# Performance work log

Hardware: AMD Instinct MI355X
Metric: run time of the kernel (lower is better)

Reference implementation:

```python
import jax, jax.numpy as jnp
import numpy as np

LN_EPS = 1e-5      # torch.nn.LayerNorm default
NORM_EPS = 1e-12   # torch F.normalize default


def _layernorm(x, gamma, beta):
    mu = jnp.mean(x, axis=-1, keepdims=True)
    var = jnp.mean(jnp.square(x - mu), axis=-1, keepdims=True)
    return (x - mu) * jax.lax.rsqrt(var + LN_EPS) * gamma + beta


def _l2norm(x):
    # normalize over last (embedding) axis, matching F.normalize(dim=1) on [B,E,1,N]
    n = jnp.sqrt(jnp.sum(jnp.square(x), axis=-1, keepdims=True))
    return x / jnp.maximum(n, NORM_EPS)


def setup_inputs() -> dict:
    key = jax.random.key(0)
    ks = jax.random.split(key, 4)
    B, N, C, E = 8, 4096, 768, 768
    x = jax.random.normal(ks[0], (B, N, C), dtype=jnp.float32)
    w_qkv = jax.random.normal(ks[1], (C, 3 * E), dtype=jnp.float32) * (1.0 / np.sqrt(C))
    w_proj = jax.random.normal(ks[2], (E, C), dtype=jnp.float32) * (1.0 / np.sqrt(E))
    ln_in_g = jnp.ones((C,), jnp.float32)
    ln_in_b = jnp.zeros((C,), jnp.float32)
    ln_out_g = jnp.ones((E,), jnp.float32)
    ln_out_b = jnp.zeros((E,), jnp.float32)
    return {"x": x, "w_qkv": w_qkv, "w_proj": w_proj,
            "ln_in_g": ln_in_g, "ln_in_b": ln_in_b,
            "ln_out_g": ln_out_g, "ln_out_b": ln_out_b}


def reference(x, w_qkv, w_proj, ln_in_g, ln_in_b, ln_out_g, ln_out_b):
    # x: [B, N, C]
    h = _layernorm(x, ln_in_g, ln_in_b)
    qkv = h @ w_qkv                                  # [B, N, 3E]
    q, k, v = jnp.split(qkv, 3, axis=-1)             # each [B, N, E]
    phi_q = _l2norm(q)                               # per-token L2 over E
    phi_k = _l2norm(k)
    kv = jnp.sum(phi_k * v, axis=1)                  # [B, E] (sum over tokens N)
    attn = phi_q * kv[:, None, :]                    # [B, N, E]
    out = _layernorm(attn, ln_out_g, ln_out_b) @ w_proj  # [B, N, C]
    return out
```

## Files before the change

### kernel.cpp

```cpp
#include <hip/hip_runtime.h>
#include <hip/hip_bf16.h>
#include <cstdint>

typedef __bf16 bf16;
typedef __bf16 bf16x4 __attribute__((ext_vector_type(4)));
typedef __bf16 bf16x8 __attribute__((ext_vector_type(8)));
typedef float f32x4 __attribute__((ext_vector_type(4)));

#define GK 768
#define LN_EPS 1e-5f
#define NORM_EPS 1e-12f

__device__ __forceinline__ void gl_lds16(const void* g, void* l) {
  __builtin_amdgcn_global_load_lds(
      (__attribute__((address_space(1))) uint32_t*)(uintptr_t)g,
      (__attribute__((address_space(3))) uint32_t*)(uintptr_t)l,
      16, 0, 0);
}

__device__ __forceinline__ void blockReduce2(float& s, float& ss, float* sm) {
  #pragma unroll
  for (int o = 32; o > 0; o >>= 1) {
    s  += __shfl_down(s, o, 64);
    ss += __shfl_down(ss, o, 64);
  }
  int wave = threadIdx.x >> 6, lane = threadIdx.x & 63;
  if (lane == 0) { sm[wave] = s; sm[4 + wave] = ss; }
  __syncthreads();
  s  = sm[0] + sm[1] + sm[2] + sm[3];
  ss = sm[4] + sm[5] + sm[6] + sm[7];
  __syncthreads();
}

__global__ __launch_bounds__(256) void transpose_cvt(const float* __restrict__ w,
                                                     bf16* __restrict__ wt,
                                                     int R, int Ncols) {
  __shared__ float tile[32][33];
  int tx = threadIdx.x & 31, ty = threadIdx.x >> 5;
  int c0 = blockIdx.x * 32, r0 = blockIdx.y * 32;
  #pragma unroll
  for (int i = 0; i < 32; i += 8)
    tile[ty + i][tx] = w[(size_t)(r0 + ty + i) * Ncols + (c0 + tx)];
  __syncthreads();
  #pragma unroll
  for (int i = 0; i < 32; i += 8)
    wt[(size_t)(c0 + ty + i) * R + (r0 + tx)] = (bf16)tile[tx][ty + i];
}

__global__ __launch_bounds__(256) void ln_in_kernel(const float* __restrict__ x,
                                                    const float* __restrict__ g,
                                                    const float* __restrict__ b,
                                                    bf16* __restrict__ h) {
  __shared__ float sm[8];
  int row = blockIdx.x, t = threadIdx.x;
  const float* xr = x + (size_t)row * 768;
  float4 v = make_float4(0.f, 0.f, 0.f, 0.f);
  if (t < 192) v = ((const float4*)xr)[t];
  float s  = v.x + v.y + v.z + v.w;
  float ss = v.x * v.x + v.y * v.y + v.z * v.z + v.w * v.w;
  blockReduce2(s, ss, sm);
  float mu  = s * (1.0f / 768.0f);
  float inv = rsqrtf(ss * (1.0f / 768.0f) - mu * mu + LN_EPS);
  if (t < 192) {
    float4 gg = ((const float4*)g)[t];
    float4 bb = ((const float4*)b)[t];
    bf16x4 o;
    o[0] = (bf16)((v.x - mu) * inv * gg.x + bb.x);
    o[1] = (bf16)((v.y - mu) * inv * gg.y + bb.y);
    o[2] = (bf16)((v.z - mu) * inv * gg.z + bb.z);
    o[3] = (bf16)((v.w - mu) * inv * gg.w + bb.w);
    ((bf16x4*)(h + (size_t)row * 768))[t] = o;
  }
}


#define SWZ(x) ((x) ^ ((((x) >> 7) & 7) << 4))

#define PH_ENTER do { __builtin_amdgcn_sched_barrier(0); __builtin_amdgcn_s_barrier(); \
                      __builtin_amdgcn_sched_barrier(0); } while (0)
#define PH_EXIT  do { __builtin_amdgcn_sched_barrier(0); __builtin_amdgcn_s_barrier(); \
                      __builtin_amdgcn_sched_barrier(0); } while (0)
#define PH_EXIT_V do { __builtin_amdgcn_sched_barrier(0); \
                       asm volatile("s_waitcnt vmcnt(4)" ::: "memory"); \
                       __builtin_amdgcn_s_barrier(); \
                       __builtin_amdgcn_sched_barrier(0); } while (0)

#define LDA1(base, mh, i, ks) \
  af[i][ks] = *(const bf16x8*)((base) + SWZ((wm * 128 + ((mh) * 4 + (i)) * 16 + llo) * 128 + (ks) * 64 + lhi * 16))
#define LDAQ(base, mh) do { \
  LDA1(base, mh, 0, 0); LDA1(base, mh, 0, 1); LDA1(base, mh, 1, 0); LDA1(base, mh, 1, 1); \
  LDA1(base, mh, 2, 0); LDA1(base, mh, 2, 1); LDA1(base, mh, 3, 0); LDA1(base, mh, 3, 1); } while (0)

#define LDB1(base, n, ks) \
  bf[n][ks] = *(const bf16x8*)((base) + SWZ(((((n) >> 1) * 128 + wn * 32 + ((n) & 1) * 16 + llo) * 128 + (ks) * 64 + lhi * 16)))
#define LDBH(base, nlo) do { \
  LDB1(base, nlo, 0); LDB1(base, nlo, 1); LDB1(base, (nlo) + 1, 0); LDB1(base, (nlo) + 1, 1); } while (0)

#define MF1(mh, nh, i, jn, ks) \
  acc[(mh) * 4 + (i)][(nh) * 2 + (jn)] = __builtin_amdgcn_mfma_f32_16x16x32_bf16( \
      af[i][ks], bf[(nh) * 2 + (jn)][ks], acc[(mh) * 4 + (i)][(nh) * 2 + (jn)], 0, 0, 0)
#define MFQ(mh, nh) do { \
  __builtin_amdgcn_s_setprio(1); \
  MF1(mh, nh, 0, 0, 0); MF1(mh, nh, 0, 1, 0); MF1(mh, nh, 1, 0, 0); MF1(mh, nh, 1, 1, 0); \
  MF1(mh, nh, 2, 0, 0); MF1(mh, nh, 2, 1, 0); MF1(mh, nh, 3, 0, 0); MF1(mh, nh, 3, 1, 0); \
  MF1(mh, nh, 0, 0, 1); MF1(mh, nh, 0, 1, 1); MF1(mh, nh, 1, 0, 1); MF1(mh, nh, 1, 1, 1); \
  MF1(mh, nh, 2, 0, 1); MF1(mh, nh, 2, 1, 1); MF1(mh, nh, 3, 0, 1); MF1(mh, nh, 3, 1, 1); \
  __builtin_amdgcn_s_setprio(0); } while (0)

#define STA(b, q, kt) gl_lds16(A + srcA[q] + (kt) * 64, &As_[b][(q) * 4096 + wave * 512])
#define STB(b, q, kt) gl_lds16(Bt + srcB[q] + (kt) * 64, &Bs_[b][(q) * 4096 + wave * 512])

template <bool OUT_BF16>
__global__ __launch_bounds__(512, 2) void gemm8p(const bf16* __restrict__ A,
                                                 const bf16* __restrict__ Bt,
                                                 void* __restrict__ Cv,
                                                 int Nn, int NBN) {
  __shared__ __align__(16) bf16 As_[2][16384];
  __shared__ __align__(16) bf16 Bs_[2][16384];
  const int tid = threadIdx.x;
  const int wave = tid >> 6, lane = tid & 63;
  const int llo = lane & 15, lhi = lane >> 4;
  const int wm = wave >> 2, wn = wave & 3;

  const int nwg = gridDim.x, bid = blockIdx.x;
  const int wg = (bid & 7) * (nwg >> 3) + (bid >> 3);
  const int rb = wg / NBN, cb = wg - rb * NBN;
  const int brow = rb * 256, bcol = cb * 256;

  uint32_t srcA[4], srcB[4];
  #pragma unroll
  for (int q = 0; q < 4; ++q) {
    int d = q * 8192 + tid * 16;
    int a = SWZ(d);
    int r = a >> 7, c = (a & 127) >> 1;
    srcA[q] = (uint32_t)(brow + r) * GK + c;
    int nh = r >> 7, wnn = (r >> 5) & 3, r32 = r & 31;
    srcB[q] = (uint32_t)(bcol + wnn * 64 + nh * 32 + r32) * GK + c;
  }

  f32x4 acc[8][4];
  #pragma unroll
  for (int m = 0; m < 8; ++m)
    #pragma unroll
    for (int n = 0; n < 4; ++n) acc[m][n] = (f32x4){0.f, 0.f, 0.f, 0.f};

  bf16x8 af[4][2], bf[4][2];
  const char* As0 = (const char*)&As_[0][0];
  const char* As1 = (const char*)&As_[1][0];
  const char* Bs0 = (const char*)&Bs_[0][0];
  const char* Bs1 = (const char*)&Bs_[1][0];

  STA(0, 0, 0); STA(0, 1, 0); STA(0, 2, 0); STA(0, 3, 0);
  STB(0, 0, 0); STB(0, 1, 0); STB(0, 2, 0); STB(0, 3, 0);
  STA(1, 0, 1); STA(1, 2, 1); STB(1, 0, 1); STB(1, 1, 1);
  __builtin_amdgcn_sched_barrier(0);
  asm volatile("s_waitcnt vmcnt(4)" ::: "memory");
  __builtin_amdgcn_s_barrier();
  __builtin_amdgcn_sched_barrier(0);

  for (int j = 0; j < 6; ++j) {
    const int t1 = 2 * j + 1, t2 = 2 * j + 2, t3 = 2 * j + 3;
    LDAQ(As0, 0); LDBH(Bs0, 0);
    STA(1, 1, t1); STA(1, 3, t1);
    PH_ENTER; MFQ(0, 0); PH_EXIT;
    LDBH(Bs0, 2);
    STB(1, 2, t1); STB(1, 3, t1);
    PH_ENTER; MFQ(0, 1); PH_EXIT;
    LDAQ(As0, 1);
    STA(0, 0, t2); STA(0, 2, t2);
    PH_ENTER; MFQ(1, 0); PH_EXIT;
    STB(0, 0, t2); STB(0, 1, t2);
    PH_ENTER; MFQ(1, 1); PH_EXIT_V;
    LDAQ(As1, 0); LDBH(Bs1, 0);
    STA(0, 1, t2); STA(0, 3, t2);
    PH_ENTER; MFQ(0, 0); PH_EXIT;
    LDBH(Bs1, 2);
    STB(0, 2, t2); STB(0, 3, t2);
    PH_ENTER; MFQ(0, 1); PH_EXIT;
    LDAQ(As1, 1);
    STA(1, 0, t3); STA(1, 2, t3);
    PH_ENTER; MFQ(1, 0); PH_EXIT;
    STB(1, 0, t3); STB(1, 1, t3);
    PH_ENTER; MFQ(1, 1); PH_EXIT_V;
  }

  #pragma unroll
  for (int m = 0; m < 8; ++m) {
    #pragma unroll
    for (int n = 0; n < 4; ++n) {
      int row = brow + wm * 128 + m * 16 + lhi * 4;
      int col = bcol + wn * 64 + n * 16 + llo;
      #pragma unroll
      for (int r2 = 0; r2 < 4; ++r2) {
        if (OUT_BF16)
          ((bf16*)Cv)[(size_t)(row + r2) * Nn + col] = (bf16)acc[m][n][r2];
        else
          ((float*)Cv)[(size_t)(row + r2) * Nn + col] = acc[m][n][r2];
      }
    }
  }
}

__global__ __launch_bounds__(256) void kv_partial(const bf16* __restrict__ qkv,
                                                  float* __restrict__ kvp) {
  __shared__ float sm[4][768];
  int b = blockIdx.x >> 5, chunk = blockIdx.x & 31;
  int wave = threadIdx.x >> 6, lane = threadIdx.x & 63;
  const bf16* base = qkv + ((size_t)(b * 4096 + chunk * 128 + wave * 32)) * 2304;
  float acc[3][4] = {};
  for (int i = 0; i < 32; ++i) {
    const bf16* kr = base + (size_t)i * 2304 + 768;
    const bf16* vr = kr + 768;
    bf16x4 k4[3], v4[3];
    #pragma unroll
    for (int c = 0; c < 3; ++c) {
      k4[c] = *(const bf16x4*)(kr + c * 256 + lane * 4);
      v4[c] = *(const bf16x4*)(vr + c * 256 + lane * 4);
    }
    float ssk = 0.f;
    #pragma unroll
    for (int c = 0; c < 3; ++c)
      #pragma unroll
      for (int j = 0; j < 4; ++j) { float kf = (float)k4[c][j]; ssk += kf * kf; }
    #pragma unroll
    for (int off = 32; off > 0; off >>= 1) ssk += __shfl_xor(ssk, off, 64);
    float wi = 1.0f / fmaxf(sqrtf(ssk), NORM_EPS);
    #pragma unroll
    for (int c = 0; c < 3; ++c)
      #pragma unroll
      for (int j = 0; j < 4; ++j)
        acc[c][j] += (float)k4[c][j] * (float)v4[c][j] * wi;
  }
  #pragma unroll
  for (int c = 0; c < 3; ++c)
    #pragma unroll
    for (int j = 0; j < 4; ++j)
      sm[wave][c * 256 + lane * 4 + j] = acc[c][j];
  __syncthreads();
  int t = threadIdx.x;
  #pragma unroll
  for (int c = 0; c < 3; ++c) {
    int e = c * 256 + t;
    kvp[(size_t)blockIdx.x * 768 + e] = sm[0][e] + sm[1][e] + sm[2][e] + sm[3][e];
  }
}

__global__ __launch_bounds__(256) void kv_reduce(const float* __restrict__ kvp,
                                                 float* __restrict__ kv) {
  int i = blockIdx.x * 256 + threadIdx.x;
  int b = i / 768, e = i - b * 768;
  float s = 0.f;
  #pragma unroll
  for (int c = 0; c < 32; ++c) s += kvp[(size_t)(b * 32 + c) * 768 + e];
  kv[i] = s;
}

__global__ __launch_bounds__(256) void attn_ln_kernel(const bf16* __restrict__ qkv,
                                                      const float* __restrict__ kv,
                                                      const float* __restrict__ g,
                                                      const float* __restrict__ b,
                                                      bf16* __restrict__ a) {
  __shared__ float sm[8];
  int row = blockIdx.x, t = threadIdx.x;
  int bt = row >> 12;
  const bf16* qr = qkv + (size_t)row * 2304;
  bf16x4 q4 = {};
  if (t < 192) q4 = ((const bf16x4*)qr)[t];
  float q0 = (float)q4[0], q1 = (float)q4[1], q2 = (float)q4[2], q3 = (float)q4[3];
  float sq = q0 * q0 + q1 * q1 + q2 * q2 + q3 * q3, dummy = 0.f;
  blockReduce2(sq, dummy, sm);
  float iq = 1.0f / fmaxf(sqrtf(sq), NORM_EPS);
  float4 av = make_float4(0.f, 0.f, 0.f, 0.f);
  if (t < 192) {
    float4 kv4 = ((const float4*)(kv + bt * 768))[t];
    av.x = q0 * iq * kv4.x;
    av.y = q1 * iq * kv4.y;
    av.z = q2 * iq * kv4.z;
    av.w = q3 * iq * kv4.w;
  }
  float s  = av.x + av.y + av.z + av.w;
  float ss = av.x * av.x + av.y * av.y + av.z * av.z + av.w * av.w;
  blockReduce2(s, ss, sm);
  float mu  = s * (1.0f / 768.0f);
  float inv = rsqrtf(ss * (1.0f / 768.0f) - mu * mu + LN_EPS);
  if (t < 192) {
    float4 gg = ((const float4*)g)[t];
    float4 bb = ((const float4*)b)[t];
    bf16x4 o;
    o[0] = (bf16)((av.x - mu) * inv * gg.x + bb.x);
    o[1] = (bf16)((av.y - mu) * inv * gg.y + bb.y);
    o[2] = (bf16)((av.z - mu) * inv * gg.z + bb.z);
    o[3] = (bf16)((av.w - mu) * inv * gg.w + bb.w);
    ((bf16x4*)(a + (size_t)row * 768))[t] = o;
  }
}

extern "C" void kernel_launch(void* const* d_in, const int* in_sizes, int n_in,
                              void* d_out, int out_size, void* d_ws, size_t ws_size,
                              hipStream_t stream) {
  const float* x      = (const float*)d_in[0];
  const float* w_qkv  = (const float*)d_in[1];
  const float* w_proj = (const float*)d_in[2];
  const float* g_in   = (const float*)d_in[3];
  const float* b_in   = (const float*)d_in[4];
  const float* g_out  = (const float*)d_in[5];
  const float* b_out  = (const float*)d_in[6];

  char* ws = (char*)d_ws;
  bf16*  wqkvt  = (bf16*)(ws);
  bf16*  wprojt = (bf16*)(ws + 3538944);
  bf16*  h      = (bf16*)(ws + 4718592);
  bf16*  qkv    = (bf16*)(ws + 55050240);
  float* kvp    = (float*)(ws + 206045184);
  float* kv     = (float*)(ws + 206831616);

  transpose_cvt<<<dim3(2304 / 32, 768 / 32), 256, 0, stream>>>(w_qkv, wqkvt, 768, 2304);
  transpose_cvt<<<dim3(768 / 32, 768 / 32), 256, 0, stream>>>(w_proj, wprojt, 768, 768);
  ln_in_kernel<<<32768, 256, 0, stream>>>(x, g_in, b_in, h);
  gemm8p<true><<<128 * 9, 512, 0, stream>>>(h, wqkvt, (void*)qkv, 2304, 9);
  kv_partial<<<256, 256, 0, stream>>>(qkv, kvp);
  kv_reduce<<<24, 256, 0, stream>>>(kvp, kv);
  attn_ln_kernel<<<32768, 256, 0, stream>>>(qkv, kv, g_out, b_out, h);
  gemm8p<false><<<128 * 3, 512, 0, stream>>>(h, wprojt, d_out, 768, 3);
}
```

Baseline: 298.5 us.

## Split GEMM phases with fine-grained lgkmcnt waits and shrink LayerNorm blocks to 192 threads

```diff
diff --git a/kernel.cpp b/kernel.cpp
--- a/kernel.cpp
+++ b/kernel.cpp
@@ -18,17 +18,17 @@
       16, 0, 0);
 }
 
-__device__ __forceinline__ void blockReduce2(float& s, float& ss, float* sm) {
+__device__ __forceinline__ void blockReduce2w3(float& s, float& ss, float* sm) {
   #pragma unroll
   for (int o = 32; o > 0; o >>= 1) {
     s  += __shfl_down(s, o, 64);
     ss += __shfl_down(ss, o, 64);
   }
   int wave = threadIdx.x >> 6, lane = threadIdx.x & 63;
-  if (lane == 0) { sm[wave] = s; sm[4 + wave] = ss; }
+  if (lane == 0) { sm[wave] = s; sm[3 + wave] = ss; }
   __syncthreads();
-  s  = sm[0] + sm[1] + sm[2] + sm[3];
-  ss = sm[4] + sm[5] + sm[6] + sm[7];
+  s  = sm[0] + sm[1] + sm[2];
+  ss = sm[3] + sm[4] + sm[5];
   __syncthreads();
 }
 
@@ -47,65 +47,51 @@
     wt[(size_t)(c0 + ty + i) * R + (r0 + tx)] = (bf16)tile[tx][ty + i];
 }
 
-__global__ __launch_bounds__(256) void ln_in_kernel(const float* __restrict__ x,
+__global__ __launch_bounds__(192) void ln_in_kernel(const float* __restrict__ x,
                                                     const float* __restrict__ g,
                                                     const float* __restrict__ b,
                                                     bf16* __restrict__ h) {
-  __shared__ float sm[8];
+  __shared__ float sm[6];
   int row = blockIdx.x, t = threadIdx.x;
   const float* xr = x + (size_t)row * 768;
-  float4 v = make_float4(0.f, 0.f, 0.f, 0.f);
-  if (t < 192) v = ((const float4*)xr)[t];
+  float4 v = ((const float4*)xr)[t];
   float s  = v.x + v.y + v.z + v.w;
   float ss = v.x * v.x + v.y * v.y + v.z * v.z + v.w * v.w;
-  blockReduce2(s, ss, sm);
+  blockReduce2w3(s, ss, sm);
   float mu  = s * (1.0f / 768.0f);
   float inv = rsqrtf(ss * (1.0f / 768.0f) - mu * mu + LN_EPS);
-  if (t < 192) {
-    float4 gg = ((const float4*)g)[t];
-    float4 bb = ((const float4*)b)[t];
-    bf16x4 o;
-    o[0] = (bf16)((v.x - mu) * inv * gg.x + bb.x);
-    o[1] = (bf16)((v.y - mu) * inv * gg.y + bb.y);
-    o[2] = (bf16)((v.z - mu) * inv * gg.z + bb.z);
-    o[3] = (bf16)((v.w - mu) * inv * gg.w + bb.w);
-    ((bf16x4*)(h + (size_t)row * 768))[t] = o;
-  }
+  float4 gg = ((const float4*)g)[t];
+  float4 bb = ((const float4*)b)[t];
+  bf16x4 o;
+  o[0] = (bf16)((v.x - mu) * inv * gg.x + bb.x);
+  o[1] = (bf16)((v.y - mu) * inv * gg.y + bb.y);
+  o[2] = (bf16)((v.z - mu) * inv * gg.z + bb.z);
+  o[3] = (bf16)((v.w - mu) * inv * gg.w + bb.w);
+  ((bf16x4*)(h + (size_t)row * 768))[t] = o;
 }
 
 
 #define SWZ(x) ((x) ^ ((((x) >> 7) & 7) << 4))
 
-#define PH_ENTER do { __builtin_amdgcn_sched_barrier(0); __builtin_amdgcn_s_barrier(); \
-                      __builtin_amdgcn_sched_barrier(0); } while (0)
-#define PH_EXIT  do { __builtin_amdgcn_sched_barrier(0); __builtin_amdgcn_s_barrier(); \
-                      __builtin_amdgcn_sched_barrier(0); } while (0)
-#define PH_EXIT_V do { __builtin_amdgcn_sched_barrier(0); \
-                       asm volatile("s_waitcnt vmcnt(4)" ::: "memory"); \
-                       __builtin_amdgcn_s_barrier(); \
-                       __builtin_amdgcn_sched_barrier(0); } while (0)
+#define SB0 __builtin_amdgcn_sched_barrier(0)
+#define BARS do { SB0; __builtin_amdgcn_s_barrier(); SB0; } while (0)
+#define LGKM(n) do { asm volatile("s_waitcnt lgkmcnt(" #n ")" ::: "memory"); SB0; } while (0)
+#define VMC4 do { SB0; asm volatile("s_waitcnt vmcnt(4)" ::: "memory"); } while (0)
+#define PRIO1 __builtin_amdgcn_s_setprio(1)
+#define PRIO0 __builtin_amdgcn_s_setprio(0)
 
 #define LDA1(base, mh, i, ks) \
   af[i][ks] = *(const bf16x8*)((base) + SWZ((wm * 128 + ((mh) * 4 + (i)) * 16 + llo) * 128 + (ks) * 64 + lhi * 16))
-#define LDAQ(base, mh) do { \
-  LDA1(base, mh, 0, 0); LDA1(base, mh, 0, 1); LDA1(base, mh, 1, 0); LDA1(base, mh, 1, 1); \
-  LDA1(base, mh, 2, 0); LDA1(base, mh, 2, 1); LDA1(base, mh, 3, 0); LDA1(base, mh, 3, 1); } while (0)
 
 #define LDB1(base, n, ks) \
   bf[n][ks] = *(const bf16x8*)((base) + SWZ(((((n) >> 1) * 128 + wn * 32 + ((n) & 1) * 16 + llo) * 128 + (ks) * 64 + lhi * 16)))
-#define LDBH(base, nlo) do { \
-  LDB1(base, nlo, 0); LDB1(base, nlo, 1); LDB1(base, (nlo) + 1, 0); LDB1(base, (nlo) + 1, 1); } while (0)
 
 #define MF1(mh, nh, i, jn, ks) \
   acc[(mh) * 4 + (i)][(nh) * 2 + (jn)] = __builtin_amdgcn_mfma_f32_16x16x32_bf16( \
       af[i][ks], bf[(nh) * 2 + (jn)][ks], acc[(mh) * 4 + (i)][(nh) * 2 + (jn)], 0, 0, 0)
-#define MFQ(mh, nh) do { \
-  __builtin_amdgcn_s_setprio(1); \
-  MF1(mh, nh, 0, 0, 0); MF1(mh, nh, 0, 1, 0); MF1(mh, nh, 1, 0, 0); MF1(mh, nh, 1, 1, 0); \
-  MF1(mh, nh, 2, 0, 0); MF1(mh, nh, 2, 1, 0); MF1(mh, nh, 3, 0, 0); MF1(mh, nh, 3, 1, 0); \
-  MF1(mh, nh, 0, 0, 1); MF1(mh, nh, 0, 1, 1); MF1(mh, nh, 1, 0, 1); MF1(mh, nh, 1, 1, 1); \
-  MF1(mh, nh, 2, 0, 1); MF1(mh, nh, 2, 1, 1); MF1(mh, nh, 3, 0, 1); MF1(mh, nh, 3, 1, 1); \
-  __builtin_amdgcn_s_setprio(0); } while (0)
+#define MF8(mh, nh, ks) do { \
+  MF1(mh, nh, 0, 0, ks); MF1(mh, nh, 0, 1, ks); MF1(mh, nh, 1, 0, ks); MF1(mh, nh, 1, 1, ks); \
+  MF1(mh, nh, 2, 0, ks); MF1(mh, nh, 2, 1, ks); MF1(mh, nh, 3, 0, ks); MF1(mh, nh, 3, 1, ks); } while (0)
 
 #define STA(b, q, kt) gl_lds16(A + srcA[q] + (kt) * 64, &As_[b][(q) * 4096 + wave * 512])
 #define STB(b, q, kt) gl_lds16(Bt + srcB[q] + (kt) * 64, &Bs_[b][(q) * 4096 + wave * 512])
@@ -153,35 +139,71 @@
   STA(0, 0, 0); STA(0, 1, 0); STA(0, 2, 0); STA(0, 3, 0);
   STB(0, 0, 0); STB(0, 1, 0); STB(0, 2, 0); STB(0, 3, 0);
   STA(1, 0, 1); STA(1, 2, 1); STB(1, 0, 1); STB(1, 1, 1);
-  __builtin_amdgcn_sched_barrier(0);
+  SB0;
   asm volatile("s_waitcnt vmcnt(4)" ::: "memory");
   __builtin_amdgcn_s_barrier();
-  __builtin_amdgcn_sched_barrier(0);
+  SB0;
 
   for (int j = 0; j < 6; ++j) {
     const int t1 = 2 * j + 1, t2 = 2 * j + 2, t3 = 2 * j + 3;
-    LDAQ(As0, 0); LDBH(Bs0, 0);
+    LDA1(As0, 0, 0, 0); LDA1(As0, 0, 1, 0); LDA1(As0, 0, 2, 0); LDA1(As0, 0, 3, 0);
+    LDB1(Bs0, 0, 0);    LDB1(Bs0, 1, 0);
+    SB0;
+    LDA1(As0, 0, 0, 1); LDA1(As0, 0, 1, 1); LDA1(As0, 0, 2, 1); LDA1(As0, 0, 3, 1);
+    LDB1(Bs0, 0, 1);    LDB1(Bs0, 1, 1);
+    SB0;
+    LDB1(Bs0, 2, 0); LDB1(Bs0, 3, 0); LDB1(Bs0, 2, 1); LDB1(Bs0, 3, 1);
     STA(1, 1, t1); STA(1, 3, t1);
-    PH_ENTER; MFQ(0, 0); PH_EXIT;
-    LDBH(Bs0, 2);
+    BARS;
+    LGKM(10); PRIO1; MF8(0, 0, 0);
+    LGKM(4);  MF8(0, 0, 1); PRIO0;
+    BARS;
     STB(1, 2, t1); STB(1, 3, t1);
-    PH_ENTER; MFQ(0, 1); PH_EXIT;
-    LDAQ(As0, 1);
+    BARS;
+    LGKM(0); PRIO1; MF8(0, 1, 0); MF8(0, 1, 1); PRIO0;
+    BARS;
+    LDA1(As0, 1, 0, 0); LDA1(As0, 1, 1, 0); LDA1(As0, 1, 2, 0); LDA1(As0, 1, 3, 0);
+    SB0;
+    LDA1(As0, 1, 0, 1); LDA1(As0, 1, 1, 1); LDA1(As0, 1, 2, 1); LDA1(As0, 1, 3, 1);
     STA(0, 0, t2); STA(0, 2, t2);
-    PH_ENTER; MFQ(1, 0); PH_EXIT;
+    BARS;
+    LGKM(4); PRIO1; MF8(1, 0, 0);
+    LGKM(0); MF8(1, 0, 1); PRIO0;
+    BARS;
     STB(0, 0, t2); STB(0, 1, t2);
-    PH_ENTER; MFQ(1, 1); PH_EXIT_V;
-    LDAQ(As1, 0); LDBH(Bs1, 0);
+    BARS;
+    PRIO1; MF8(1, 1, 0); MF8(1, 1, 1); PRIO0;
+    VMC4;
+    BARS;
+    LDA1(As1, 0, 0, 0); LDA1(As1, 0, 1, 0); LDA1(As1, 0, 2, 0); LDA1(As1, 0, 3, 0);
+    LDB1(Bs1, 0, 0);    LDB1(Bs1, 1, 0);
+    SB0;
+    LDA1(As1, 0, 0, 1); LDA1(As1, 0, 1, 1); LDA1(As1, 0, 2, 1); LDA1(As1, 0, 3, 1);
+    LDB1(Bs1, 0, 1);    LDB1(Bs1, 1, 1);
+    SB0;
+    LDB1(Bs1, 2, 0); LDB1(Bs1, 3, 0); LDB1(Bs1, 2, 1); LDB1(Bs1, 3, 1);
     STA(0, 1, t2); STA(0, 3, t2);
-    PH_ENTER; MFQ(0, 0); PH_EXIT;
-    LDBH(Bs1, 2);
+    BARS;
+    LGKM(10); PRIO1; MF8(0, 0, 0);
+    LGKM(4);  MF8(0, 0, 1); PRIO0;
+    BARS;
     STB(0, 2, t2); STB(0, 3, t2);
-    PH_ENTER; MFQ(0, 1); PH_EXIT;
-    LDAQ(As1, 1);
+    BARS;
+    LGKM(0); PRIO1; MF8(0, 1, 0); MF8(0, 1, 1); PRIO0;
+    BARS;
+    LDA1(As1, 1, 0, 0); LDA1(As1, 1, 1, 0); LDA1(As1, 1, 2, 0); LDA1(As1, 1, 3, 0);
+    SB0;
+    LDA1(As1, 1, 0, 1); LDA1(As1, 1, 1, 1); LDA1(As1, 1, 2, 1); LDA1(As1, 1, 3, 1);
     STA(1, 0, t3); STA(1, 2, t3);
-    PH_ENTER; MFQ(1, 0); PH_EXIT;
+    BARS;
+    LGKM(4); PRIO1; MF8(1, 0, 0);
+    LGKM(0); MF8(1, 0, 1); PRIO0;
+    BARS;
     STB(1, 0, t3); STB(1, 1, t3);
-    PH_ENTER; MFQ(1, 1); PH_EXIT_V;
+    BARS;
+    PRIO1; MF8(1, 1, 0); MF8(1, 1, 1); PRIO0;
+    VMC4;
+    BARS;
   }
 
   #pragma unroll
@@ -255,44 +277,39 @@
   kv[i] = s;
 }
 
-__global__ __launch_bounds__(256) void attn_ln_kernel(const bf16* __restrict__ qkv,
+__global__ __launch_bounds__(192) void attn_ln_kernel(const bf16* __restrict__ qkv,
                                                       const float* __restrict__ kv,
                                                       const float* __restrict__ g,
                                                       const float* __restrict__ b,
                                                       bf16* __restrict__ a) {
-  __shared__ float sm[8];
+  __shared__ float sm[6];
   int row = blockIdx.x, t = threadIdx.x;
   int bt = row >> 12;
   const bf16* qr = qkv + (size_t)row * 2304;
-  bf16x4 q4 = {};
-  if (t < 192) q4 = ((const bf16x4*)qr)[t];
+  bf16x4 q4 = ((const bf16x4*)qr)[t];
   float q0 = (float)q4[0], q1 = (float)q4[1], q2 = (float)q4[2], q3 = (float)q4[3];
   float sq = q0 * q0 + q1 * q1 + q2 * q2 + q3 * q3, dummy = 0.f;
-  blockReduce2(sq, dummy, sm);
+  blockReduce2w3(sq, dummy, sm);
   float iq = 1.0f / fmaxf(sqrtf(sq), NORM_EPS);
-  float4 av = make_float4(0.f, 0.f, 0.f, 0.f);
-  if (t < 192) {
-    float4 kv4 = ((const float4*)(kv + bt * 768))[t];
-    av.x = q0 * iq * kv4.x;
-    av.y = q1 * iq * kv4.y;
-    av.z = q2 * iq * kv4.z;
-    av.w = q3 * iq * kv4.w;
-  }
+  float4 kv4 = ((const float4*)(kv + bt * 768))[t];
+  float4 av;
+  av.x = q0 * iq * kv4.x;
+  av.y = q1 * iq * kv4.y;
+  av.z = q2 * iq * kv4.z;
+  av.w = q3 * iq * kv4.w;
   float s  = av.x + av.y + av.z + av.w;
   float ss = av.x * av.x + av.y * av.y + av.z * av.z + av.w * av.w;
-  blockReduce2(s, ss, sm);
+  blockReduce2w3(s, ss, sm);
   float mu  = s * (1.0f / 768.0f);
   float inv = rsqrtf(ss * (1.0f / 768.0f) - mu * mu + LN_EPS);
-  if (t < 192) {
-    float4 gg = ((const float4*)g)[t];
-    float4 bb = ((const float4*)b)[t];
-    bf16x4 o;
-    o[0] = (bf16)((av.x - mu) * inv * gg.x + bb.x);
-    o[1] = (bf16)((av.y - mu) * inv * gg.y + bb.y);
-    o[2] = (bf16)((av.z - mu) * inv * gg.z + bb.z);
-    o[3] = (bf16)((av.w - mu) * inv * gg.w + bb.w);
-    ((bf16x4*)(a + (size_t)row * 768))[t] = o;
-  }
+  float4 gg = ((const float4*)g)[t];
+  float4 bb = ((const float4*)b)[t];
+  bf16x4 o;
+  o[0] = (bf16)((av.x - mu) * inv * gg.x + bb.x);
+  o[1] = (bf16)((av.y - mu) * inv * gg.y + bb.y);
+  o[2] = (bf16)((av.z - mu) * inv * gg.z + bb.z);
+  o[3] = (bf16)((av.w - mu) * inv * gg.w + bb.w);
+  ((bf16x4*)(a + (size_t)row * 768))[t] = o;
 }
 
 extern "C" void kernel_launch(void* const* d_in, const int* in_sizes, int n_in,
@@ -316,10 +333,10 @@
 
   transpose_cvt<<<dim3(2304 / 32, 768 / 32), 256, 0, stream>>>(w_qkv, wqkvt, 768, 2304);
   transpose_cvt<<<dim3(768 / 32, 768 / 32), 256, 0, stream>>>(w_proj, wprojt, 768, 768);
-  ln_in_kernel<<<32768, 256, 0, stream>>>(x, g_in, b_in, h);
+  ln_in_kernel<<<32768, 192, 0, stream>>>(x, g_in, b_in, h);
   gemm8p<true><<<128 * 9, 512, 0, stream>>>(h, wqkvt, (void*)qkv, 2304, 9);
   kv_partial<<<256, 256, 0, stream>>>(qkv, kvp);
   kv_reduce<<<24, 256, 0, stream>>>(kvp, kv);
-  attn_ln_kernel<<<32768, 256, 0, stream>>>(qkv, kv, g_out, b_out, h);
+  attn_ln_kernel<<<32768, 192, 0, stream>>>(qkv, kv, g_out, b_out, h);
   gemm8p<false><<<128 * 3, 512, 0, stream>>>(h, wprojt, d_out, 768, 3);
 }
```

Result: faster. 292.6 us (-2.0%).
